# Kernel optimization log

Hardware: AMD Instinct MI355X
Metric: run time of the kernel (lower is better)

## Reference

```python
import jax, jax.numpy as jnp
import numpy as np

N_NODES = 100000
N_EDGES = 1600000
IN_FEATS = 128
N_HIDDEN = 128
N_CLASSES = 47


def setup_inputs() -> dict:
    key = jax.random.key(0)
    ks = jax.random.split(key, 9)
    x = jax.random.normal(ks[0], (N_NODES, IN_FEATS), dtype=jnp.float32)
    src = jax.random.randint(ks[1], (N_EDGES,), 0, N_NODES, dtype=jnp.int32)
    dst = jax.random.randint(ks[2], (N_EDGES,), 0, N_NODES, dtype=jnp.int32)
    s = 0.05
    return {
        "x": x, "src": src, "dst": dst,
        "Ws0": jax.random.normal(ks[3], (IN_FEATS, N_HIDDEN), jnp.float32) * s,
        "Wn0": jax.random.normal(ks[4], (IN_FEATS, N_HIDDEN), jnp.float32) * s,
        "b0": jnp.zeros((N_HIDDEN,), jnp.float32),
        "Ws1": jax.random.normal(ks[5], (N_HIDDEN, N_HIDDEN), jnp.float32) * s,
        "Wn1": jax.random.normal(ks[6], (N_HIDDEN, N_HIDDEN), jnp.float32) * s,
        "b1": jnp.zeros((N_HIDDEN,), jnp.float32),
        "Ws2": jax.random.normal(ks[7], (N_HIDDEN, N_CLASSES), jnp.float32) * s,
        "Wn2": jax.random.normal(ks[8], (N_HIDDEN, N_CLASSES), jnp.float32) * s,
        "b2": jnp.zeros((N_CLASSES,), jnp.float32),
    }


def _sage_layer(h, src, dst, inv_deg, Ws, Wn, b):
    # weighted (w=1) mean aggregation over in-neighbors: sum(h[src]) / in_degree
    msg = h[src]  # [E, d] irregular gather
    neigh = jax.ops.segment_sum(msg, dst, num_segments=N_NODES) * inv_deg[:, None]
    # DGL SAGEConv 'mean': fc_self(h_self) + fc_neigh(h_neigh), bias on self branch
    return h @ Ws + neigh @ Wn + b


def reference(x, src, dst, Ws0, Wn0, b0, Ws1, Wn1, b1, Ws2, Wn2, b2):
    deg = jax.ops.segment_sum(jnp.ones_like(dst, dtype=x.dtype), dst, num_segments=N_NODES)
    inv_deg = 1.0 / jnp.maximum(deg, 1.0)
    h = _sage_layer(x, src, dst, inv_deg, Ws0, Wn0, b0)
    h = jax.nn.relu(h)  # dropout is identity (eval / p=0)
    h = _sage_layer(h, src, dst, inv_deg, Ws1, Wn1, b1)
    h = jax.nn.relu(h)
    h = _sage_layer(h, src, dst, inv_deg, Ws2, Wn2, b2)
    return jax.nn.log_softmax(h, axis=-1)
```

## Files before the change

### kernel.cpp

```cpp
#include <hip/hip_runtime.h>
#include <hip/hip_bf16.h>

#define NN 100000
#define NE 1600000
#define F 128
#define NCLS 47

#define NPB 256
#define BUCKETS 391
#define ABLK 512
#define ACHUNK (NE / ABLK)

typedef __attribute__((ext_vector_type(8))) short short8;
typedef __attribute__((ext_vector_type(8))) unsigned short u16x8;
typedef __attribute__((ext_vector_type(4))) float f32x4;

#define MFMA16(A, B, C) __builtin_amdgcn_mfma_f32_16x16x32_bf16(A, B, C, 0, 0, 0)

__device__ __forceinline__ unsigned short b16(float f) {
    unsigned int u = __builtin_bit_cast(unsigned int, f);
    unsigned int r = u + 0x7FFFu + ((u >> 16) & 1u);
    return (unsigned short)(r >> 16);
}
__device__ __forceinline__ float bflo(unsigned int u) { return __builtin_bit_cast(float, u << 16); }
__device__ __forceinline__ float bfhi(unsigned int u) { return __builtin_bit_cast(float, u & 0xFFFF0000u); }

__global__ void __launch_bounds__(256) k_bhist(const int* __restrict__ dst,
                                               int* __restrict__ bucket_cnt) {
    __shared__ int hist[BUCKETS];
    const int t = threadIdx.x;
    for (int i = t; i < BUCKETS; i += 256) hist[i] = 0;
    __syncthreads();
    const int e0 = blockIdx.x * ACHUNK;
    for (int i = t; i < ACHUNK; i += 256) atomicAdd(&hist[dst[e0 + i] >> 8], 1);
    __syncthreads();
    for (int i = t; i < BUCKETS; i += 256)
        if (hist[i]) atomicAdd(&bucket_cnt[i], hist[i]);
}

__global__ void k_bscan(const int* __restrict__ bucket_cnt, int* __restrict__ bucket_off,
                        int* __restrict__ cursor) {
    const int lane = threadIdx.x & 63;
    int run = 0;
#pragma unroll
    for (int c = 0; c < 7; c++) {
        int idx = c * 64 + lane;
        int v = (idx < BUCKETS) ? bucket_cnt[idx] : 0;
        int s = v;
#pragma unroll
        for (int off = 1; off < 64; off <<= 1) {
            int n = __shfl_up(s, off);
            if (lane >= off) s += n;
        }
        int excl = run + s - v;
        if (idx <= BUCKETS) {
            bucket_off[idx] = excl;
            cursor[idx] = excl;
        }
        run += __shfl(s, 63);
    }
}

__global__ void __launch_bounds__(256) k_bscatter(const int* __restrict__ src,
                                                  const int* __restrict__ dst,
                                                  int* __restrict__ cursor,
                                                  unsigned int* __restrict__ ebuf) {
    __shared__ int hist[BUCKETS];
    __shared__ int base[BUCKETS];
    __shared__ int rank[BUCKETS];
    const int t = threadIdx.x;
    for (int i = t; i < BUCKETS; i += 256) {
        hist[i] = 0;
        rank[i] = 0;
    }
    __syncthreads();
    const int e0 = blockIdx.x * ACHUNK;
    for (int i = t; i < ACHUNK; i += 256) atomicAdd(&hist[dst[e0 + i] >> 8], 1);
    __syncthreads();
    for (int i = t; i < BUCKETS; i += 256) {
        int h = hist[i];
        base[i] = h ? atomicAdd(&cursor[i], h) : 0;
    }
    __syncthreads();
    for (int i = t; i < ACHUNK; i += 256) {
        unsigned int s = (unsigned int)src[e0 + i];
        int d = dst[e0 + i];
        int b = d >> 8;
        int r = atomicAdd(&rank[b], 1);
        ebuf[base[b] + r] = s | ((unsigned int)(d & 255) << 24);
    }
}

__global__ void __launch_bounds__(256) k_bcsr(const unsigned int* __restrict__ ebuf,
                                              const int* __restrict__ bucket_off,
                                              int* __restrict__ row_off,
                                              float* __restrict__ inv_deg,
                                              int* __restrict__ col) {
    __shared__ int cnt[NPB];
    __shared__ int ro[NPB];
    __shared__ int wsum[4];
    const int t = threadIdx.x, lane = t & 63, wid = t >> 6;
    cnt[t] = 0;
    __syncthreads();
    const int e0 = bucket_off[blockIdx.x], e1 = bucket_off[blockIdx.x + 1];
    for (int i = e0 + t; i < e1; i += 256) atomicAdd(&cnt[ebuf[i] >> 24], 1);
    __syncthreads();
    int v = cnt[t];
    int run = v;
#pragma unroll
    for (int off = 1; off < 64; off <<= 1) {
        int n = __shfl_up(run, off);
        if (lane >= off) run += n;
    }
    if (lane == 63) wsum[wid] = run;
    __syncthreads();
    int woff = e0;
#pragma unroll
    for (int wv = 0; wv < 4; wv++)
        if (wv < wid) woff += wsum[wv];
    int excl = woff + run - v;
    int node = (blockIdx.x << 8) + t;
    if (node < NN) {
        row_off[node] = excl;
        inv_deg[node] = 1.0f / fmaxf((float)v, 1.0f);
    }
    if (blockIdx.x == BUCKETS - 1 && t == 0) row_off[NN] = NE;
    ro[t] = excl;
    cnt[t] = 0;
    __syncthreads();
    for (int i = e0 + t; i < e1; i += 256) {
        unsigned int e = ebuf[i];
        int d = e >> 24;
        int p = atomicAdd(&cnt[d], 1);
        col[ro[d] + p] = (int)(e & 0xFFFFFFu);
    }
}

__global__ void k_cvt(const float* __restrict__ x, unsigned short* __restrict__ xb) {
    int t = blockIdx.x * blockDim.x + threadIdx.x;
    if (t >= NN * F / 8) return;
    const float4* x4 = (const float4*)x;
    float4 a = x4[t * 2], b = x4[t * 2 + 1];
    u16x8 o;
    o[0] = b16(a.x); o[1] = b16(a.y); o[2] = b16(a.z); o[3] = b16(a.w);
    o[4] = b16(b.x); o[5] = b16(b.y); o[6] = b16(b.z); o[7] = b16(b.w);
    ((u16x8*)xb)[t] = o;
}

__global__ void k_zpad(unsigned short* __restrict__ xb, unsigned short* __restrict__ h1b,
                       unsigned short* __restrict__ hw2b) {
    int t = threadIdx.x;
    xb[(size_t)NN * F + t] = 0;
    h1b[(size_t)NN * F + t] = 0;
    if (t < 64) hw2b[(size_t)NN * 64 + t] = 0;
}

__global__ void k_pack_all(const float* __restrict__ Ws0, const float* __restrict__ Wn0,
                           const float* __restrict__ Ws1, const float* __restrict__ Wn1,
                           const float* __restrict__ Ws2, const float* __restrict__ Wn2,
                           unsigned short* __restrict__ wp) {
    int idx = blockIdx.x * blockDim.x + threadIdx.x;
    if (idx >= 77824) return;
    const float* W;
    int base, ncols;
    if (idx < 65536) {
        int m = idx >> 14;
        W = (m == 0) ? Ws0 : (m == 1) ? Wn0 : (m == 2) ? Ws1 : Wn1;
        base = m << 14;
        ncols = 128;
    } else {
        int m = (idx - 65536) / 6144;
        W = m ? Wn2 : Ws2;
        base = 65536 + m * 6144;
        ncols = NCLS;
    }
    int li = idx - base;
    int nt = li >> 11;
    int r = li & 2047;
    int kk = r >> 9;
    int r2 = r & 511;
    int lane = r2 >> 3;
    int j = r2 & 7;
    int k = kk * 32 + ((lane >> 4) << 3) + j;
    int n = nt * 16 + (lane & 15);
    float v = (n < ncols) ? W[k * ncols + n] : 0.f;
    wp[idx] = b16(v);
}

__global__ void __launch_bounds__(256) k_aggbh(const uint4* __restrict__ h4,
                                               const int* __restrict__ row_off,
                                               const int* __restrict__ col,
                                               const float* __restrict__ inv_deg,
                                               uint4* __restrict__ a4) {
    const int bI = blockIdx.x;
    const int xcd = bI & 7;
    const int half = xcd >> 2;
    const int bh = (bI >> 3) * 4 + (xcd & 3);
    const int wid = threadIdx.x >> 6, lane = threadIdx.x & 63;
    const int node = bh * 4 + wid;
    if (node >= NN) return;
    const int hoff = half * 8;
    int b = row_off[node], e = row_off[node + 1];
    int deg = e - b;
    const int g = lane >> 3, fl = lane & 7;
    float acc[8];
#pragma unroll
    for (int i = 0; i < 8; i++) acc[i] = 0.f;
    for (int base = 0; base < deg; base += 64) {
        int cnt = deg - base;
        if (cnt > 64) cnt = 64;
        int myc = col[b + base + (lane < cnt ? lane : 0)];
        for (int jj = 0; jj < cnt; jj += 16) {
            uint4 u[2];
#pragma unroll
            for (int k2 = 0; k2 < 2; k2++) {
                int r = jj + k2 * 8 + g;
                int c = __shfl(myc, r);
                c = (r < cnt) ? c : NN;
                u[k2] = h4[(size_t)(unsigned)c * 16u + hoff + fl];
            }
#pragma unroll
            for (int k2 = 0; k2 < 2; k2++) {
                uint4 v = u[k2];
                acc[0] += bflo(v.x); acc[1] += bfhi(v.x);
                acc[2] += bflo(v.y); acc[3] += bfhi(v.y);
                acc[4] += bflo(v.z); acc[5] += bfhi(v.z);
                acc[6] += bflo(v.w); acc[7] += bfhi(v.w);
            }
        }
    }
#pragma unroll
    for (int i = 0; i < 8; i++) {
        acc[i] += __shfl_xor(acc[i], 8);
        acc[i] += __shfl_xor(acc[i], 16);
        acc[i] += __shfl_xor(acc[i], 32);
    }
    if (lane < 8) {
        float s = inv_deg[node];
        uint4 o;
        o.x = (unsigned)b16(acc[0] * s) | ((unsigned)b16(acc[1] * s) << 16);
        o.y = (unsigned)b16(acc[2] * s) | ((unsigned)b16(acc[3] * s) << 16);
        o.z = (unsigned)b16(acc[4] * s) | ((unsigned)b16(acc[5] * s) << 16);
        o.w = (unsigned)b16(acc[6] * s) | ((unsigned)b16(acc[7] * s) << 16);
        a4[(size_t)node * 16 + hoff + fl] = o;
    }
}

__global__ void __launch_bounds__(256) k_agg48(const uint4* __restrict__ hw4,
                                               const int* __restrict__ row_off,
                                               const int* __restrict__ col,
                                               const float* __restrict__ inv_deg,
                                               uint4* __restrict__ aggh4) {
    int node = (blockIdx.x * blockDim.x + threadIdx.x) >> 6;
    int lane = threadIdx.x & 63;
    if (node >= NN) return;
    int b = row_off[node], e = row_off[node + 1];
    int deg = e - b;
    const int g = lane >> 3, fl = lane & 7;
    float acc[8];
#pragma unroll
    for (int i = 0; i < 8; i++) acc[i] = 0.f;
    for (int base = 0; base < deg; base += 64) {
        int cnt = deg - base;
        if (cnt > 64) cnt = 64;
        int myc = col[b + base + (lane < cnt ? lane : 0)];
        for (int jj = 0; jj < cnt; jj += 16) {
            uint4 u[2];
#pragma unroll
            for (int k2 = 0; k2 < 2; k2++) {
                int r = jj + k2 * 8 + g;
                int c = __shfl(myc, r);
                c = (r < cnt) ? c : NN;
                u[k2] = hw4[(size_t)(unsigned)c * 8u + fl];
            }
#pragma unroll
            for (int k2 = 0; k2 < 2; k2++) {
                uint4 v = u[k2];
                acc[0] += bflo(v.x); acc[1] += bfhi(v.x);
                acc[2] += bflo(v.y); acc[3] += bfhi(v.y);
                acc[4] += bflo(v.z); acc[5] += bfhi(v.z);
                acc[6] += bflo(v.w); acc[7] += bfhi(v.w);
            }
        }
    }
#pragma unroll
    for (int i = 0; i < 8; i++) {
        acc[i] += __shfl_xor(acc[i], 8);
        acc[i] += __shfl_xor(acc[i], 16);
        acc[i] += __shfl_xor(acc[i], 32);
    }
    if (lane < 8) {
        float s = inv_deg[node];
        uint4 o;
        o.x = (unsigned)b16(acc[0] * s) | ((unsigned)b16(acc[1] * s) << 16);
        o.y = (unsigned)b16(acc[2] * s) | ((unsigned)b16(acc[3] * s) << 16);
        o.z = (unsigned)b16(acc[4] * s) | ((unsigned)b16(acc[5] * s) << 16);
        o.w = (unsigned)b16(acc[6] * s) | ((unsigned)b16(acc[7] * s) << 16);
        aggh4[(size_t)node * 8 + fl] = o;
    }
}

template <bool RELU>
__global__ void __launch_bounds__(256) k_layer(const unsigned short* __restrict__ hb,
                                               const unsigned short* __restrict__ ab,
                                               const unsigned short* __restrict__ wps,
                                               const unsigned short* __restrict__ wpn,
                                               const float* __restrict__ bias,
                                               unsigned short* __restrict__ outb) {
    const int wid = threadIdx.x >> 6, lane = threadIdx.x & 63;
    const int tile0 = blockIdx.x * 64;
    const short8* ws8 = (const short8*)wps;
    const short8* wn8 = (const short8*)wpn;
    short8 wf[2][2][4];
#pragma unroll
    for (int t = 0; t < 2; t++) {
        int nt = 2 * wid + t;
#pragma unroll
        for (int kk = 0; kk < 4; kk++) {
            wf[0][t][kk] = ws8[(nt * 4 + kk) * 64 + lane];
            wf[1][t][kk] = wn8[(nt * 4 + kk) * 64 + lane];
        }
    }
    const int rb = lane & 15, kq = lane >> 4;
    float bv[2];
#pragma unroll
    for (int t = 0; t < 2; t++) bv[t] = bias[(2 * wid + t) * 16 + rb];
    const short8* h8 = (const short8*)hb;
    const short8* a8 = (const short8*)ab;
    f32x4 zero = {0.f, 0.f, 0.f, 0.f};
    f32x4 acc[4][2];
#pragma unroll
    for (int m = 0; m < 4; m++)
#pragma unroll
        for (int t = 0; t < 2; t++) acc[m][t] = zero;
#pragma unroll
    for (int kk = 0; kk < 4; kk++) {
#pragma unroll
        for (int m = 0; m < 4; m++) {
            int row = tile0 + m * 16 + rb;
            int rc = row < NN ? row : NN - 1;
            int idx = rc * 16 + kk * 4 + kq;
            short8 af = h8[idx];
            short8 gf = a8[idx];
            acc[m][0] = MFMA16(af, wf[0][0][kk], acc[m][0]);
            acc[m][1] = MFMA16(af, wf[0][1][kk], acc[m][1]);
            acc[m][0] = MFMA16(gf, wf[1][0][kk], acc[m][0]);
            acc[m][1] = MFMA16(gf, wf[1][1][kk], acc[m][1]);
        }
    }
#pragma unroll
    for (int m = 0; m < 4; m++) {
#pragma unroll
        for (int reg = 0; reg < 4; reg++) {
            int row = tile0 + m * 16 + kq * 4 + reg;
            if (row < NN) {
#pragma unroll
                for (int t = 0; t < 2; t++) {
                    float v = acc[m][t][reg] + bv[t];
                    if (RELU) v = fmaxf(v, 0.f);
                    outb[(size_t)row * F + (2 * wid + t) * 16 + rb] = b16(v);
                }
            }
        }
    }
}

__global__ void __launch_bounds__(512) k_nmul(const unsigned short* __restrict__ hb,
                                              const unsigned short* __restrict__ wpn,
                                              unsigned short* __restrict__ hw) {
    const int wid = threadIdx.x >> 6, lane = threadIdx.x & 63;
    const int R0 = blockIdx.x * 128 + wid * 16;
    const short8* wn8 = (const short8*)wpn;
    short8 wf[3][4];
#pragma unroll
    for (int nt = 0; nt < 3; nt++)
#pragma unroll
        for (int kk = 0; kk < 4; kk++) wf[nt][kk] = wn8[(nt * 4 + kk) * 64 + lane];
    const int rb = lane & 15, kq = lane >> 4;
    const short8* h8 = (const short8*)hb;
    f32x4 zero = {0.f, 0.f, 0.f, 0.f};
    f32x4 acc[3] = {zero, zero, zero};
    int rowr = R0 + rb;
    int rc = rowr < NN ? rowr : NN - 1;
#pragma unroll
    for (int kk = 0; kk < 4; kk++) {
        short8 af = h8[rc * 16 + kk * 4 + kq];
#pragma unroll
        for (int nt = 0; nt < 3; nt++) acc[nt] = MFMA16(af, wf[nt][kk], acc[nt]);
    }
#pragma unroll
    for (int reg = 0; reg < 4; reg++) {
        int row = R0 + kq * 4 + reg;
        if (row < NN) {
#pragma unroll
            for (int nt = 0; nt < 3; nt++)
                hw[(size_t)row * 64 + nt * 16 + rb] = b16(acc[nt][reg]);
        }
    }
}

__global__ void __launch_bounds__(512) k_out2(const unsigned short* __restrict__ hb,
                                              const unsigned short* __restrict__ aggh,
                                              const unsigned short* __restrict__ wps,
                                              const float* __restrict__ bias,
                                              float* __restrict__ out) {
    const int wid = threadIdx.x >> 6, lane = threadIdx.x & 63;
    const int R0 = blockIdx.x * 128 + wid * 16;
    const short8* ws8 = (const short8*)wps;
    short8 wf[3][4];
#pragma unroll
    for (int nt = 0; nt < 3; nt++)
#pragma unroll
        for (int kk = 0; kk < 4; kk++) wf[nt][kk] = ws8[(nt * 4 + kk) * 64 + lane];
    const int rb = lane & 15, kq = lane >> 4;
    float bv[3];
    bool valid[3];
#pragma unroll
    for (int nt = 0; nt < 3; nt++) {
        int c = nt * 16 + rb;
        valid[nt] = c < NCLS;
        bv[nt] = valid[nt] ? bias[c] : 0.f;
    }
    const short8* h8 = (const short8*)hb;
    f32x4 zero = {0.f, 0.f, 0.f, 0.f};
    f32x4 acc[3] = {zero, zero, zero};
    int rowr = R0 + rb;
    int rc = rowr < NN ? rowr : NN - 1;
#pragma unroll
    for (int kk = 0; kk < 4; kk++) {
        short8 af = h8[rc * 16 + kk * 4 + kq];
#pragma unroll
        for (int nt = 0; nt < 3; nt++) acc[nt] = MFMA16(af, wf[nt][kk], acc[nt]);
    }
#pragma unroll
    for (int reg = 0; reg < 4; reg++) {
        int row = R0 + kq * 4 + reg;
        int rc2 = row < NN ? row : NN - 1;
        float v[3];
        float mx = -1e30f;
#pragma unroll
        for (int nt = 0; nt < 3; nt++) {
            float av = __builtin_bit_cast(
                float, (unsigned)aggh[(size_t)rc2 * 64 + nt * 16 + rb] << 16);
            v[nt] = acc[nt][reg] + av + bv[nt];
            if (valid[nt]) mx = fmaxf(mx, v[nt]);
        }
        for (int off = 1; off < 16; off <<= 1) mx = fmaxf(mx, __shfl_xor(mx, off));
        float s = 0.f;
#pragma unroll
        for (int nt = 0; nt < 3; nt++)
            if (valid[nt]) s += expf(v[nt] - mx);
        for (int off = 1; off < 16; off <<= 1) s += __shfl_xor(s, off);
        float L = mx + logf(s);
        if (row < NN) {
#pragma unroll
            for (int nt = 0; nt < 3; nt++)
                if (valid[nt]) out[(size_t)row * NCLS + nt * 16 + rb] = v[nt] - L;
        }
    }
}

extern "C" void kernel_launch(void* const* d_in, const int* in_sizes, int n_in,
                              void* d_out, int out_size, void* d_ws, size_t ws_size,
                              hipStream_t stream) {
    (void)in_sizes; (void)n_in; (void)out_size; (void)ws_size;
    const float* x = (const float*)d_in[0];
    const int* src = (const int*)d_in[1];
    const int* dst = (const int*)d_in[2];
    const float* Ws0 = (const float*)d_in[3];
    const float* Wn0 = (const float*)d_in[4];
    const float* b0 = (const float*)d_in[5];
    const float* Ws1 = (const float*)d_in[6];
    const float* Wn1 = (const float*)d_in[7];
    const float* b1 = (const float*)d_in[8];
    const float* Ws2 = (const float*)d_in[9];
    const float* Wn2 = (const float*)d_in[10];
    const float* b2 = (const float*)d_in[11];
    float* out = (float*)d_out;

    char* w = (char*)d_ws;
    size_t off = 0;
    auto alloc = [&](size_t bytes) -> char* {
        char* p = w + off;
        off = (off + bytes + 255) & ~(size_t)255;
        return p;
    };
    int* row_off = (int*)alloc((size_t)(NN + 1) * 4);
    int* col = (int*)alloc((size_t)NE * 4);
    float* inv_deg = (float*)alloc((size_t)NN * 4);
    int* bucket_cnt = (int*)alloc((size_t)(BUCKETS + 1) * 4);
    int* bucket_off = (int*)alloc((size_t)(BUCKETS + 1) * 4);
    int* bcursor = (int*)alloc((size_t)(BUCKETS + 1) * 4);
    unsigned int* ebuf = (unsigned int*)alloc((size_t)(NN + 1) * 64 * 2);
    unsigned short* xb = (unsigned short*)alloc((size_t)(NN + 1) * F * 2);
    unsigned short* aggb = (unsigned short*)alloc((size_t)NN * F * 2);
    unsigned short* h1b = (unsigned short*)alloc((size_t)(NN + 1) * F * 2);
    unsigned short* h2b = (unsigned short*)alloc((size_t)NN * F * 2);
    unsigned short* wp = (unsigned short*)alloc((size_t)77824 * 2);

    unsigned short* hw2b = (unsigned short*)ebuf;
    unsigned short* aggh = aggb;

    hipMemsetAsync(bucket_cnt, 0, (size_t)(BUCKETS + 1) * 4, stream);

    k_bhist<<<ABLK, 256, 0, stream>>>(dst, bucket_cnt);
    k_bscan<<<1, 64, 0, stream>>>(bucket_cnt, bucket_off, bcursor);
    k_bscatter<<<ABLK, 256, 0, stream>>>(src, dst, bcursor, ebuf);
    k_bcsr<<<BUCKETS, 256, 0, stream>>>(ebuf, bucket_off, row_off, inv_deg, col);

    k_cvt<<<(NN * F / 8 + 255) / 256, 256, 0, stream>>>(x, xb);
    k_pack_all<<<(77824 + 255) / 256, 256, 0, stream>>>(Ws0, Wn0, Ws1, Wn1, Ws2, Wn2, wp);

    unsigned short* wS0 = wp;
    unsigned short* wN0 = wp + 16384;
    unsigned short* wS1 = wp + 32768;
    unsigned short* wN1 = wp + 49152;
    unsigned short* wS2 = wp + 65536;
    unsigned short* wN2 = wp + 71680;

    const int AGGH_B = 50000;
    const int AGG_B = NN * 64 / 256;
    const int LYR_B = (NN + 63) / 64;
    const int OUT_B = (NN + 127) / 128;

    k_zpad<<<1, 128, 0, stream>>>(xb, h1b, hw2b);

    k_aggbh<<<AGGH_B, 256, 0, stream>>>((const uint4*)xb, row_off, col, inv_deg, (uint4*)aggb);
    k_layer<true><<<LYR_B, 256, 0, stream>>>(xb, aggb, wS0, wN0, b0, h1b);
    k_aggbh<<<AGGH_B, 256, 0, stream>>>((const uint4*)h1b, row_off, col, inv_deg, (uint4*)aggb);
    k_layer<true><<<LYR_B, 256, 0, stream>>>(h1b, aggb, wS1, wN1, b1, h2b);
    k_nmul<<<OUT_B, 512, 0, stream>>>(h2b, wN2, hw2b);
    k_agg48<<<AGG_B, 256, 0, stream>>>((const uint4*)hw2b, row_off, col, inv_deg,
                                       (uint4*)aggh);
    k_out2<<<OUT_B, 512, 0, stream>>>(h2b, aggh, wS2, b2, out);
}
```

Before: 360.1 us.

## Aggregate full feature rows per wave instead of XCD-split half rows; fold zero-pad into cvt

Replaces the half-row aggregation kernel, which split each node's 128 features across two XCD halves with one wave per node-half, with a kernel where one wave gathers the full 256-byte row using 16 lanes per neighbor and 4 neighbors per step. This halves the number of blocks and the index and row_off reads. It drops the XCD-aware mapping that was meant to keep each half of the feature table resident in separate L2 caches, so L2 locality may get worse. The separate zero-pad kernel launch is also folded into the conversion kernel.

```diff
diff --git a/kernel.cpp b/kernel.cpp
--- a/kernel.cpp
+++ b/kernel.cpp
@@ -136,8 +136,17 @@
     }
 }
 
-__global__ void k_cvt(const float* __restrict__ x, unsigned short* __restrict__ xb) {
+__global__ void k_cvt(const float* __restrict__ x, unsigned short* __restrict__ xb,
+                      unsigned short* __restrict__ h1b, unsigned short* __restrict__ hw2b) {
     int t = blockIdx.x * blockDim.x + threadIdx.x;
+    if (blockIdx.x == 0) {
+        int tt = threadIdx.x;
+        if (tt < 128) {
+            xb[(size_t)NN * F + tt] = 0;
+            h1b[(size_t)NN * F + tt] = 0;
+            if (tt < 64) hw2b[(size_t)NN * 64 + tt] = 0;
+        }
+    }
     if (t >= NN * F / 8) return;
     const float4* x4 = (const float4*)x;
     float4 a = x4[t * 2], b = x4[t * 2 + 1];
@@ -145,14 +154,6 @@
     o[0] = b16(a.x); o[1] = b16(a.y); o[2] = b16(a.z); o[3] = b16(a.w);
     o[4] = b16(b.x); o[5] = b16(b.y); o[6] = b16(b.z); o[7] = b16(b.w);
     ((u16x8*)xb)[t] = o;
-}
-
-__global__ void k_zpad(unsigned short* __restrict__ xb, unsigned short* __restrict__ h1b,
-                       unsigned short* __restrict__ hw2b) {
-    int t = threadIdx.x;
-    xb[(size_t)NN * F + t] = 0;
-    h1b[(size_t)NN * F + t] = 0;
-    if (t < 64) hw2b[(size_t)NN * 64 + t] = 0;
 }
 
 __global__ void k_pack_all(const float* __restrict__ Ws0, const float* __restrict__ Wn0,
@@ -187,22 +188,17 @@
     wp[idx] = b16(v);
 }
 
-__global__ void __launch_bounds__(256) k_aggbh(const uint4* __restrict__ h4,
-                                               const int* __restrict__ row_off,
-                                               const int* __restrict__ col,
-                                               const float* __restrict__ inv_deg,
-                                               uint4* __restrict__ a4) {
-    const int bI = blockIdx.x;
-    const int xcd = bI & 7;
-    const int half = xcd >> 2;
-    const int bh = (bI >> 3) * 4 + (xcd & 3);
-    const int wid = threadIdx.x >> 6, lane = threadIdx.x & 63;
-    const int node = bh * 4 + wid;
+__global__ void __launch_bounds__(256) k_aggb(const uint4* __restrict__ h4,
+                                              const int* __restrict__ row_off,
+                                              const int* __restrict__ col,
+                                              const float* __restrict__ inv_deg,
+                                              uint4* __restrict__ a4) {
+    int node = (blockIdx.x * blockDim.x + threadIdx.x) >> 6;
+    int lane = threadIdx.x & 63;
     if (node >= NN) return;
-    const int hoff = half * 8;
     int b = row_off[node], e = row_off[node + 1];
     int deg = e - b;
-    const int g = lane >> 3, fl = lane & 7;
+    const int g = lane >> 4, fl = lane & 15;
     float acc[8];
 #pragma unroll
     for (int i = 0; i < 8; i++) acc[i] = 0.f;
@@ -211,16 +207,16 @@
         if (cnt > 64) cnt = 64;
         int myc = col[b + base + (lane < cnt ? lane : 0)];
         for (int jj = 0; jj < cnt; jj += 16) {
-            uint4 u[2];
-#pragma unroll
-            for (int k2 = 0; k2 < 2; k2++) {
-                int r = jj + k2 * 8 + g;
+            uint4 u[4];
+#pragma unroll
+            for (int k2 = 0; k2 < 4; k2++) {
+                int r = jj + k2 * 4 + g;
                 int c = __shfl(myc, r);
                 c = (r < cnt) ? c : NN;
-                u[k2] = h4[(size_t)(unsigned)c * 16u + hoff + fl];
+                u[k2] = h4[(size_t)(unsigned)c * 16u + fl];
             }
 #pragma unroll
-            for (int k2 = 0; k2 < 2; k2++) {
+            for (int k2 = 0; k2 < 4; k2++) {
                 uint4 v = u[k2];
                 acc[0] += bflo(v.x); acc[1] += bfhi(v.x);
                 acc[2] += bflo(v.y); acc[3] += bfhi(v.y);
@@ -231,18 +227,17 @@
     }
 #pragma unroll
     for (int i = 0; i < 8; i++) {
-        acc[i] += __shfl_xor(acc[i], 8);
         acc[i] += __shfl_xor(acc[i], 16);
         acc[i] += __shfl_xor(acc[i], 32);
     }
-    if (lane < 8) {
+    if (g == 0) {
         float s = inv_deg[node];
         uint4 o;
         o.x = (unsigned)b16(acc[0] * s) | ((unsigned)b16(acc[1] * s) << 16);
         o.y = (unsigned)b16(acc[2] * s) | ((unsigned)b16(acc[3] * s) << 16);
         o.z = (unsigned)b16(acc[4] * s) | ((unsigned)b16(acc[5] * s) << 16);
         o.w = (unsigned)b16(acc[6] * s) | ((unsigned)b16(acc[7] * s) << 16);
-        a4[(size_t)node * 16 + hoff + fl] = o;
+        a4[(size_t)node * 16 + fl] = o;
     }
 }
 
@@ -508,7 +503,7 @@
     k_bscatter<<<ABLK, 256, 0, stream>>>(src, dst, bcursor, ebuf);
     k_bcsr<<<BUCKETS, 256, 0, stream>>>(ebuf, bucket_off, row_off, inv_deg, col);
 
-    k_cvt<<<(NN * F / 8 + 255) / 256, 256, 0, stream>>>(x, xb);
+    k_cvt<<<(NN * F / 8 + 255) / 256, 256, 0, stream>>>(x, xb, h1b, hw2b);
     k_pack_all<<<(77824 + 255) / 256, 256, 0, stream>>>(Ws0, Wn0, Ws1, Wn1, Ws2, Wn2, wp);
 
     unsigned short* wS0 = wp;
@@ -518,16 +513,13 @@
     unsigned short* wS2 = wp + 65536;
     unsigned short* wN2 = wp + 71680;
 
-    const int AGGH_B = 50000;
     const int AGG_B = NN * 64 / 256;
     const int LYR_B = (NN + 63) / 64;
     const int OUT_B = (NN + 127) / 128;
 
-    k_zpad<<<1, 128, 0, stream>>>(xb, h1b, hw2b);
-
-    k_aggbh<<<AGGH_B, 256, 0, stream>>>((const uint4*)xb, row_off, col, inv_deg, (uint4*)aggb);
+    k_aggb<<<AGG_B, 256, 0, stream>>>((const uint4*)xb, row_off, col, inv_deg, (uint4*)aggb);
     k_layer<true><<<LYR_B, 256, 0, stream>>>(xb, aggb, wS0, wN0, b0, h1b);
-    k_aggbh<<<AGGH_B, 256, 0, stream>>>((const uint4*)h1b, row_off, col, inv_deg, (uint4*)aggb);
+    k_aggb<<<AGG_B, 256, 0, stream>>>((const uint4*)h1b, row_off, col, inv_deg, (uint4*)aggb);
     k_layer<true><<<LYR_B, 256, 0, stream>>>(h1b, aggb, wS1, wN1, b1, h2b);
     k_nmul<<<OUT_B, 512, 0, stream>>>(h2b, wN2, hw2b);
     k_agg48<<<AGG_B, 256, 0, stream>>>((const uint4*)hw2b, row_off, col, inv_deg,
```

Measured after the change: 321.8 us. 1.12x faster.
